# Kernel optimization log

Hardware: AMD Instinct MI355X
Metric: run time of the kernel (lower is better)

The kernel has to match this reference:

```python
import jax, jax.numpy as jnp
import numpy as np

# Constructor constants (from init_kwargs)
B, F, K, D = 4096, 2048, 64, 8
VOL_TEMP = 0.5   # SoftVolume temperature -> softplus beta = 1/VOL_TEMP
INT_TEMP = 0.1   # GumbelIntersection temperature
EPS = 1e-23      # box_embeddings soft-volume clamp


def setup_inputs() -> dict:
    key = jax.random.key(0)
    ks = jax.random.split(key, 9)
    def lin(k, shp, fan_in):
        return (jax.random.normal(k, shp, jnp.float32) / np.sqrt(fan_in)).astype(jnp.float32)
    return {
        "features": jax.random.normal(ks[0], (B, F), jnp.float32),
        # stacked per-concept projectors: Linear(F -> 2D) for each of K concepts
        "Wp": lin(ks[1], (K, F, 2 * D), F),
        "bp": lin(ks[2], (K, 2 * D), F),
        # stacked per-concept prob predictors: Linear(2D -> 1)
        "Wprob": lin(ks[3], (K, 2 * D), 2 * D),
        "bprob": lin(ks[4], (K,), 2 * D),
        # classifier heads
        "Wbox": lin(ks[5], (K * 2 * D, 1), K * 2 * D),
        "bbox": lin(ks[6], (1,), K * 2 * D),
        "Wrel": lin(ks[7], (K * K, 1), K * K),
        "brel": lin(ks[8], (1,), K * K),
    }


def _log_soft_volume(z, Z):
    # box_embeddings SoftVolume: sum_d log(max(softplus(Z - z, beta=1/vol_temp), eps))
    beta = 1.0 / VOL_TEMP
    side = jax.nn.softplus(beta * (Z - z)) / beta
    return jnp.sum(jnp.log(jnp.maximum(side, EPS)), axis=-1)


def reference(features, Wp, bp, Wprob, bprob, Wbox, bbox, Wrel, brel):
    b = features.shape[0]
    # all K projectors as one batched GEMM: [B,F] x [K,F,2D] -> [B,K,2D]
    theta = jnp.einsum('bf,kfd->bkd', features, Wp) + bp
    theta = theta.reshape(b, K, 2, D)
    # MinDeltaBoxTensor: z = theta[...,0,:], Z = z + softplus(theta[...,1,:])
    z = theta[:, :, 0, :]                       # [B,K,D]
    Z = z + jax.nn.softplus(theta[:, :, 1, :])  # [B,K,D]

    coords = jnp.concatenate([z, Z], axis=-1)   # [B,K,2D]
    logits = jnp.einsum('bkd,kd->bk', coords, Wprob) + bprob
    concept_probs = jax.nn.sigmoid(logits)      # [B,K]

    # Pairwise Gumbel intersection over all (i,j) concept pairs (vectorized k^2 loop)
    t = INT_TEMP
    zi, zj = z[:, :, None, :], z[:, None, :, :]   # [B,K,1,D] vs [B,1,K,D]
    Zi, Zj = Z[:, :, None, :], Z[:, None, :, :]
    z_int = t * jnp.logaddexp(zi / t, zj / t)
    z_int = jnp.maximum(z_int, jnp.maximum(zi, zj))
    Z_int = -t * jnp.logaddexp(-Zi / t, -Zj / t)
    Z_int = jnp.minimum(Z_int, jnp.minimum(Zi, Zj))

    lv_int = _log_soft_volume(z_int, Z_int)       # [B,K,K]
    lv_box = _log_soft_volume(z, Z)               # [B,K]
    # P(i|j) = vol(i ^ j) / vol(j)
    cond = jnp.clip(jnp.exp(lv_int - lv_box[:, None, :]), 1e-6, 1.0 - 1e-6)  # [B,K,K]

    # scale each box's coords by its concept prob, flatten as [z_i, Z_i] per concept
    p = concept_probs[:, :, None]
    flat_boxes = jnp.concatenate([z * p, Z * p], axis=-1).reshape(b, K * 2 * D)
    flat_rel = cond.reshape(b, K * K)

    final_logit = flat_boxes @ Wbox + bbox + flat_rel @ Wrel + brel  # [B,1]
    task_probs = jax.nn.sigmoid(final_logit)
    return task_probs, concept_probs, cond
```

## Files before the change

kernel.cpp:

```cpp
#include <hip/hip_runtime.h>
#include <cstdint>
#include <cstddef>


typedef __bf16 bf16_t;
typedef __bf16 bf16x4 __attribute__((ext_vector_type(4)));
typedef __bf16 bf16x8 __attribute__((ext_vector_type(8)));
typedef float floatx4 __attribute__((ext_vector_type(4)));

#define LOG2E 1.4426950408889634f
#define LN2 0.6931471805599453f
#define K1C 14.426950408889634f
#define K3C 2.8853900817779268f

__device__ __forceinline__ float ex2(float x) { return __builtin_exp2f(x); }
__device__ __forceinline__ float lg2(float x) { return __builtin_log2f(x); }

__global__ __launch_bounds__(256, 2) void prep_b(const float* __restrict__ Wp,
                                                 bf16_t* __restrict__ Bt) {
  __shared__ float tile[128][17];
  const int kc = blockIdx.x;
  const int f0 = blockIdx.y * 128;
  const int t = threadIdx.x;
  {
    const int fl = t >> 1, dh = (t & 1) * 8;
    const float* g = Wp + ((size_t)kc * 2048 + f0 + fl) * 16 + dh;
    float4 v0 = *reinterpret_cast<const float4*>(g);
    float4 v1 = *reinterpret_cast<const float4*>(g + 4);
    tile[fl][dh + 0] = v0.x; tile[fl][dh + 1] = v0.y;
    tile[fl][dh + 2] = v0.z; tile[fl][dh + 3] = v0.w;
    tile[fl][dh + 4] = v1.x; tile[fl][dh + 5] = v1.y;
    tile[fl][dh + 6] = v1.z; tile[fl][dh + 7] = v1.w;
  }
  __syncthreads();
  {
    const int d = t >> 4, fi = (t & 15) * 8;
    float x[8];
#pragma unroll
    for (int u = 0; u < 8; ++u) x[u] = tile[fi + u][d];
    bf16x8 hv, lv;
#pragma unroll
    for (int u = 0; u < 8; ++u) {
      __bf16 h = (__bf16)x[u];
      hv[u] = h;
      lv[u] = (__bf16)(x[u] - (float)h);
    }
    const size_t row = (size_t)(kc * 16 + d) * 4096;
    *reinterpret_cast<bf16x8*>(Bt + row + f0 + fi) = hv;
    *reinterpret_cast<bf16x8*>(Bt + row + 2048 + f0 + fi) = lv;
  }
}

__global__ __launch_bounds__(256, 2) void gemm_theta(
    const float* __restrict__ A, const bf16_t* __restrict__ Bt,
    const float* __restrict__ bias, float* __restrict__ C) {
  __shared__ bf16_t Ah[128][40];
  __shared__ bf16_t Al[128][40];
  __shared__ bf16_t Bh[64][40];
  __shared__ bf16_t Bl[64][40];
  const int t = threadIdx.x;
  const int m0 = blockIdx.x * 128, n0 = blockIdx.y * 64;
  const int wave = t >> 6, lane = t & 63, quad = lane >> 4, l16 = lane & 15;
  const int wm = (wave >> 1) * 64, wn = (wave & 1) * 32;
  floatx4 acc[4][2] = {};
  const int rB = t >> 2, cB = (t & 3) * 8;

  for (int kk = 0; kk < 64; ++kk) {
    const int k = kk * 32;
#pragma unroll
    for (int q = 0; q < 4; ++q) {
      const int idx = q * 256 + t;
      const int r = idx >> 3, c4 = (idx & 7) * 4;
      const float4 v = *reinterpret_cast<const float4*>(
          A + (size_t)(m0 + r) * 2048 + k + c4);
      bf16x4 hv = {(__bf16)v.x, (__bf16)v.y, (__bf16)v.z, (__bf16)v.w};
      bf16x4 lv = {(__bf16)(v.x - (float)hv[0]), (__bf16)(v.y - (float)hv[1]),
                   (__bf16)(v.z - (float)hv[2]), (__bf16)(v.w - (float)hv[3])};
      *reinterpret_cast<bf16x4*>(&Ah[r][c4]) = hv;
      *reinterpret_cast<bf16x4*>(&Al[r][c4]) = lv;
    }
    {
      const bf16_t* src = Bt + (size_t)(n0 + rB) * 4096 + k + cB;
      *reinterpret_cast<bf16x8*>(&Bh[rB][cB]) =
          *reinterpret_cast<const bf16x8*>(src);
      *reinterpret_cast<bf16x8*>(&Bl[rB][cB]) =
          *reinterpret_cast<const bf16x8*>(src + 2048);
    }
    __syncthreads();
    bf16x8 ah[4], al[4], bh[2], bl[2];
#pragma unroll
    for (int r = 0; r < 4; ++r) {
      ah[r] = *reinterpret_cast<const bf16x8*>(&Ah[wm + r * 16 + l16][quad * 8]);
      al[r] = *reinterpret_cast<const bf16x8*>(&Al[wm + r * 16 + l16][quad * 8]);
    }
#pragma unroll
    for (int c = 0; c < 2; ++c) {
      bh[c] = *reinterpret_cast<const bf16x8*>(&Bh[wn + c * 16 + l16][quad * 8]);
      bl[c] = *reinterpret_cast<const bf16x8*>(&Bl[wn + c * 16 + l16][quad * 8]);
    }
#pragma unroll
    for (int r = 0; r < 4; ++r)
#pragma unroll
      for (int c = 0; c < 2; ++c) {
        acc[r][c] =
            __builtin_amdgcn_mfma_f32_16x16x32_bf16(ah[r], bh[c], acc[r][c], 0, 0, 0);
        acc[r][c] =
            __builtin_amdgcn_mfma_f32_16x16x32_bf16(al[r], bh[c], acc[r][c], 0, 0, 0);
        acc[r][c] =
            __builtin_amdgcn_mfma_f32_16x16x32_bf16(ah[r], bl[c], acc[r][c], 0, 0, 0);
      }
    __syncthreads();
  }
#pragma unroll
  for (int r = 0; r < 4; ++r) {
    const int row0 = m0 + wm + r * 16 + quad * 4;
#pragma unroll
    for (int c = 0; c < 2; ++c) {
      const int col = n0 + wn + c * 16 + l16;
      const float bb = bias[col];
#pragma unroll
      for (int i = 0; i < 4; ++i)
        C[(size_t)(row0 + i) * 1024 + col] = acc[r][c][i] + bb;
    }
  }
}

__global__ __launch_bounds__(256, 2) void fused_pair(
    const float* __restrict__ Th, const float* __restrict__ Wprob,
    const float* __restrict__ bprob, const float* __restrict__ Wbox,
    const float* __restrict__ bbox, const float* __restrict__ Wrel,
    const float* __restrict__ brel, float* __restrict__ out) {
  __shared__ float sboxes[64][17];
  __shared__ float spinv[64];
  __shared__ float spc[64];
  __shared__ float swrel[4096];
  __shared__ float swbox[1024];
  __shared__ float sprod[2080];
  __shared__ float sred[4];

  const int b = blockIdx.x;
  const int t = threadIdx.x;
  const float* th = Th + (size_t)b * 1024;
  float* out_task = out;
  float* out_conc = out + 4096;
  float* out_cond = out + 266240;

  if (t < 64) {
    const int k = t;
    const float* thk = th + k * 16;
    float4 a0 = reinterpret_cast<const float4*>(thk)[0];
    float4 a1 = reinterpret_cast<const float4*>(thk)[1];
    float4 a2 = reinterpret_cast<const float4*>(thk)[2];
    float4 a3 = reinterpret_cast<const float4*>(thk)[3];
    float z[8] = {a0.x, a0.y, a0.z, a0.w, a1.x, a1.y, a1.z, a1.w};
    float w1[8] = {a2.x, a2.y, a2.z, a2.w, a3.x, a3.y, a3.z, a3.w};
    float dp = 1.0f;
    float logit = bprob[k];
#pragma unroll
    for (int d = 0; d < 8; ++d) {
      const float spv = LN2 * lg2(1.0f + ex2(w1[d] * LOG2E));
      const float Zd = z[d] + spv;
      const float denl = lg2(1.0f + ex2((Zd - z[d]) * K3C));
      dp *= denl;
      logit += z[d] * Wprob[k * 16 + d] + Zd * Wprob[k * 16 + 8 + d];
      sboxes[k][d] = z[d];
      sboxes[k][8 + d] = Zd;
    }
    spinv[k] = 1.0f / dp;
    const float pk = 1.0f / (1.0f + ex2(-logit * LOG2E));
    spc[k] = pk;
    out_conc[(size_t)b * 64 + k] = pk;
  }
#pragma unroll
  for (int q = 0; q < 4; ++q)
    reinterpret_cast<float4*>(swrel)[q * 256 + t] =
        reinterpret_cast<const float4*>(Wrel)[q * 256 + t];
  reinterpret_cast<float4*>(swbox)[t] = reinterpret_cast<const float4*>(Wbox)[t];
  __syncthreads();

#pragma unroll
  for (int q = 0; q < 9; ++q) {
    const int p = t + 256 * q;
    if (p < 2080) {
      int j = (int)((sqrtf((float)(8 * p + 1)) - 1.0f) * 0.5f);
      if ((j + 1) * (j + 2) / 2 <= p) ++j;
      if (j * (j + 1) / 2 > p) --j;
      const int i = p - j * (j + 1) / 2;
      float prodn = 1.0f;
#pragma unroll
      for (int d = 0; d < 8; ++d) {
        const float zi = sboxes[i][d], Zi = sboxes[i][8 + d];
        const float zjd = sboxes[j][d], Zjd = sboxes[j][8 + d];
        const float u = ex2(-fabsf(zi - zjd) * K1C);
        const float uZ = ex2(-fabsf(Zi - Zjd) * K1C);
        const float lsum = lg2(fmaf(u, uZ, 1.0f + u + uZ));
        const float gap = fminf(Zi, Zjd) - fmaxf(zi, zjd);
        const float E = ex2(fmaf(gap, K3C, -0.2f * lsum));
        prodn *= lg2(1.0f + E);
      }
      sprod[p] = prodn;
    }
  }
  __syncthreads();

  const int wv = t >> 6, lane = t & 63;
  const float pinvj = spinv[lane];
  float rsum = 0.0f;
#pragma unroll 4
  for (int ii = 0; ii < 16; ++ii) {
    const int i = wv * 16 + ii;
    const int lo = min(i, lane), hi = max(i, lane);
    const float prodn = sprod[hi * (hi + 1) / 2 + lo];
    float cond = prodn * pinvj;
    cond = fminf(fmaxf(cond, 1e-6f), 1.0f - 1e-6f);
    out_cond[(size_t)b * 4096 + i * 64 + lane] = cond;
    rsum = fmaf(cond, swrel[i * 64 + lane], rsum);
  }

  float bsum = 0.0f;
#pragma unroll
  for (int q = 0; q < 4; ++q) {
    const int idx = t + 256 * q;
    const int k = idx >> 4, c = idx & 15;
    bsum = fmaf(sboxes[k][c] * spc[k], swbox[idx], bsum);
  }
  float total = rsum + bsum;
#pragma unroll
  for (int off = 32; off > 0; off >>= 1) total += __shfl_down(total, off, 64);
  if (lane == 0) sred[wv] = total;
  __syncthreads();
  if (t == 0) {
    const float s = sred[0] + sred[1] + sred[2] + sred[3] + bbox[0] + brel[0];
    out_task[b] = 1.0f / (1.0f + ex2(-s * LOG2E));
  }
}

extern "C" void kernel_launch(void* const* d_in, const int* in_sizes, int n_in,
                              void* d_out, int out_size, void* d_ws, size_t ws_size,
                              hipStream_t stream) {
  const float* feat = (const float*)d_in[0];
  const float* Wp = (const float*)d_in[1];
  const float* bp = (const float*)d_in[2];
  const float* Wprob = (const float*)d_in[3];
  const float* bprob = (const float*)d_in[4];
  const float* Wbox = (const float*)d_in[5];
  const float* bbox = (const float*)d_in[6];
  const float* Wrel = (const float*)d_in[7];
  const float* brel = (const float*)d_in[8];
  float* out = (float*)d_out;

  char* ws = (char*)d_ws;
  bf16_t* Bt = (bf16_t*)ws;
  float* Th = (float*)(ws + (size_t)(8 << 20));

  prep_b<<<dim3(64, 16), 256, 0, stream>>>(Wp, Bt);
  gemm_theta<<<dim3(32, 16), 256, 0, stream>>>(feat, Bt, bp, Th);
  fused_pair<<<4096, 256, 0, stream>>>(Th, Wprob, bprob, Wbox, bbox, Wrel, brel, out);
}
```

Before: 288.6 us.

## Pre-split features to bf16 and double-buffer GEMM with direct global-to-LDS loads

Adds a prep kernel that splits the fp32 features into bf16 high/low arrays once, so the GEMM no longer converts A on every tile. The GEMM now uses global_load_lds to stream A and B tiles straight into a double-buffered LDS ring, prefetching the next k-slice while MFMAs run on the current one. The N tile doubles to 128 per block, giving a 4x4 accumulator per wave, with one block per CU. It costs an extra pass over features plus more workspace. The unpadded LDS layout may also cause bank conflicts.

```diff
diff --git a/kernel.cpp b/kernel.cpp
--- a/kernel.cpp
+++ b/kernel.cpp
@@ -15,6 +15,30 @@
 
 __device__ __forceinline__ float ex2(float x) { return __builtin_exp2f(x); }
 __device__ __forceinline__ float lg2(float x) { return __builtin_log2f(x); }
+
+__device__ __forceinline__ void gload16(const bf16_t* g, bf16_t* l) {
+  __builtin_amdgcn_global_load_lds(
+      (const __attribute__((address_space(1))) void*)g,
+      (__attribute__((address_space(3))) void*)l, 16, 0, 0);
+}
+
+__global__ __launch_bounds__(256) void prep_a(const float* __restrict__ A,
+                                              bf16_t* __restrict__ Ah,
+                                              bf16_t* __restrict__ Al) {
+  const size_t i = ((size_t)blockIdx.x * 256 + threadIdx.x) * 8;
+  const float4 v0 = *reinterpret_cast<const float4*>(A + i);
+  const float4 v1 = *reinterpret_cast<const float4*>(A + i + 4);
+  const float x[8] = {v0.x, v0.y, v0.z, v0.w, v1.x, v1.y, v1.z, v1.w};
+  bf16x8 h, l;
+#pragma unroll
+  for (int u = 0; u < 8; ++u) {
+    const __bf16 hv = (__bf16)x[u];
+    h[u] = hv;
+    l[u] = (__bf16)(x[u] - (float)hv);
+  }
+  *reinterpret_cast<bf16x8*>(Ah + i) = h;
+  *reinterpret_cast<bf16x8*>(Al + i) = l;
+}
 
 __global__ __launch_bounds__(256, 2) void prep_b(const float* __restrict__ Wp,
                                                  bf16_t* __restrict__ Bt) {
@@ -51,71 +75,76 @@
   }
 }
 
-__global__ __launch_bounds__(256, 2) void gemm_theta(
-    const float* __restrict__ A, const bf16_t* __restrict__ Bt,
-    const float* __restrict__ bias, float* __restrict__ C) {
-  __shared__ bf16_t Ah[128][40];
-  __shared__ bf16_t Al[128][40];
-  __shared__ bf16_t Bh[64][40];
-  __shared__ bf16_t Bl[64][40];
+__global__ __launch_bounds__(256, 1) void gemm_theta(
+    const bf16_t* __restrict__ Ahg, const bf16_t* __restrict__ Alg,
+    const bf16_t* __restrict__ Bt, const float* __restrict__ bias,
+    float* __restrict__ C) {
+  __shared__ bf16_t lds[2][4][128 * 32];
   const int t = threadIdx.x;
-  const int m0 = blockIdx.x * 128, n0 = blockIdx.y * 64;
+  const int m0 = blockIdx.x * 128, n0 = blockIdx.y * 128;
   const int wave = t >> 6, lane = t & 63, quad = lane >> 4, l16 = lane & 15;
-  const int wm = (wave >> 1) * 64, wn = (wave & 1) * 32;
-  floatx4 acc[4][2] = {};
-  const int rB = t >> 2, cB = (t & 3) * 8;
-
+  const int wm = (wave >> 1) * 64, wn = (wave & 1) * 64;
+  floatx4 acc[4][4] = {};
+
+  const int srow = t >> 2, c8 = (t & 3) * 8;
+  const bf16_t* gAh0 = Ahg + (size_t)(m0 + srow) * 2048 + c8;
+  const bf16_t* gAh1 = Ahg + (size_t)(m0 + 64 + srow) * 2048 + c8;
+  const bf16_t* gAl0 = Alg + (size_t)(m0 + srow) * 2048 + c8;
+  const bf16_t* gAl1 = Alg + (size_t)(m0 + 64 + srow) * 2048 + c8;
+  const bf16_t* gBh0 = Bt + (size_t)(n0 + srow) * 4096 + c8;
+  const bf16_t* gBh1 = Bt + (size_t)(n0 + 64 + srow) * 4096 + c8;
+
+  auto stage = [&](int bf, int kk) {
+    const int ko = kk * 32;
+    gload16(gAh0 + ko, &lds[bf][0][t * 8]);
+    gload16(gAh1 + ko, &lds[bf][0][(256 + t) * 8]);
+    gload16(gAl0 + ko, &lds[bf][1][t * 8]);
+    gload16(gAl1 + ko, &lds[bf][1][(256 + t) * 8]);
+    gload16(gBh0 + ko, &lds[bf][2][t * 8]);
+    gload16(gBh1 + ko, &lds[bf][2][(256 + t) * 8]);
+    gload16(gBh0 + 2048 + ko, &lds[bf][3][t * 8]);
+    gload16(gBh1 + 2048 + ko, &lds[bf][3][(256 + t) * 8]);
+  };
+
+  stage(0, 0);
+  __syncthreads();
+
+  int buf = 0;
   for (int kk = 0; kk < 64; ++kk) {
-    const int k = kk * 32;
-#pragma unroll
-    for (int q = 0; q < 4; ++q) {
-      const int idx = q * 256 + t;
-      const int r = idx >> 3, c4 = (idx & 7) * 4;
-      const float4 v = *reinterpret_cast<const float4*>(
-          A + (size_t)(m0 + r) * 2048 + k + c4);
-      bf16x4 hv = {(__bf16)v.x, (__bf16)v.y, (__bf16)v.z, (__bf16)v.w};
-      bf16x4 lv = {(__bf16)(v.x - (float)hv[0]), (__bf16)(v.y - (float)hv[1]),
-                   (__bf16)(v.z - (float)hv[2]), (__bf16)(v.w - (float)hv[3])};
-      *reinterpret_cast<bf16x4*>(&Ah[r][c4]) = hv;
-      *reinterpret_cast<bf16x4*>(&Al[r][c4]) = lv;
-    }
-    {
-      const bf16_t* src = Bt + (size_t)(n0 + rB) * 4096 + k + cB;
-      *reinterpret_cast<bf16x8*>(&Bh[rB][cB]) =
-          *reinterpret_cast<const bf16x8*>(src);
-      *reinterpret_cast<bf16x8*>(&Bl[rB][cB]) =
-          *reinterpret_cast<const bf16x8*>(src + 2048);
-    }
-    __syncthreads();
-    bf16x8 ah[4], al[4], bh[2], bl[2];
+    if (kk < 63) stage(buf ^ 1, kk + 1);
+    bf16x8 ah[4], al[4], bh[4], bl[4];
 #pragma unroll
     for (int r = 0; r < 4; ++r) {
-      ah[r] = *reinterpret_cast<const bf16x8*>(&Ah[wm + r * 16 + l16][quad * 8]);
-      al[r] = *reinterpret_cast<const bf16x8*>(&Al[wm + r * 16 + l16][quad * 8]);
-    }
-#pragma unroll
-    for (int c = 0; c < 2; ++c) {
-      bh[c] = *reinterpret_cast<const bf16x8*>(&Bh[wn + c * 16 + l16][quad * 8]);
-      bl[c] = *reinterpret_cast<const bf16x8*>(&Bl[wn + c * 16 + l16][quad * 8]);
+      const int off = (wm + r * 16 + l16) * 32 + quad * 8;
+      ah[r] = *reinterpret_cast<const bf16x8*>(&lds[buf][0][off]);
+      al[r] = *reinterpret_cast<const bf16x8*>(&lds[buf][1][off]);
+    }
+#pragma unroll
+    for (int c = 0; c < 4; ++c) {
+      const int off = (wn + c * 16 + l16) * 32 + quad * 8;
+      bh[c] = *reinterpret_cast<const bf16x8*>(&lds[buf][2][off]);
+      bl[c] = *reinterpret_cast<const bf16x8*>(&lds[buf][3][off]);
     }
 #pragma unroll
     for (int r = 0; r < 4; ++r)
 #pragma unroll
-      for (int c = 0; c < 2; ++c) {
-        acc[r][c] =
-            __builtin_amdgcn_mfma_f32_16x16x32_bf16(ah[r], bh[c], acc[r][c], 0, 0, 0);
-        acc[r][c] =
-            __builtin_amdgcn_mfma_f32_16x16x32_bf16(al[r], bh[c], acc[r][c], 0, 0, 0);
-        acc[r][c] =
-            __builtin_amdgcn_mfma_f32_16x16x32_bf16(ah[r], bl[c], acc[r][c], 0, 0, 0);
+      for (int c = 0; c < 4; ++c) {
+        acc[r][c] = __builtin_amdgcn_mfma_f32_16x16x32_bf16(ah[r], bh[c],
+                                                            acc[r][c], 0, 0, 0);
+        acc[r][c] = __builtin_amdgcn_mfma_f32_16x16x32_bf16(al[r], bh[c],
+                                                            acc[r][c], 0, 0, 0);
+        acc[r][c] = __builtin_amdgcn_mfma_f32_16x16x32_bf16(ah[r], bl[c],
+                                                            acc[r][c], 0, 0, 0);
       }
     __syncthreads();
-  }
+    buf ^= 1;
+  }
+
 #pragma unroll
   for (int r = 0; r < 4; ++r) {
     const int row0 = m0 + wm + r * 16 + quad * 4;
 #pragma unroll
-    for (int c = 0; c < 2; ++c) {
+    for (int c = 0; c < 4; ++c) {
       const int col = n0 + wn + c * 16 + l16;
       const float bb = bias[col];
 #pragma unroll
@@ -252,8 +281,11 @@
   char* ws = (char*)d_ws;
   bf16_t* Bt = (bf16_t*)ws;
   float* Th = (float*)(ws + (size_t)(8 << 20));
-
+  bf16_t* Ah = (bf16_t*)(ws + (size_t)(24 << 20));
+  bf16_t* Al = (bf16_t*)(ws + (size_t)(40 << 20));
+
+  prep_a<<<4096, 256, 0, stream>>>(feat, Ah, Al);
   prep_b<<<dim3(64, 16), 256, 0, stream>>>(Wp, Bt);
-  gemm_theta<<<dim3(32, 16), 256, 0, stream>>>(feat, Bt, bp, Th);
+  gemm_theta<<<dim3(32, 8), 256, 0, stream>>>(Ah, Al, Bt, bp, Th);
   fused_pair<<<4096, 256, 0, stream>>>(Th, Wprob, bprob, Wbox, bbox, Wrel, brel, out);
 }
```

After: 281.3 us. 1.03x faster.
